# Optimization experiments

Measured on AMD Instinct MI355X. Metric: run time of the kernel, lower is better.

Reference implementation:

```python
import jax, jax.numpy as jnp
import numpy as np

N, E, IN, HID, OUT = 40000, 640000, 128, 512, 256


def setup_inputs() -> dict:
    key = jax.random.key(0)
    ks = jax.random.split(key, 8)
    x = jax.random.normal(ks[0], (N, IN), dtype=jnp.float32)
    edge_index = jax.random.randint(ks[1], (2, E), 0, N, dtype=jnp.int64)
    # SAGEConv params: lin_l (applied to aggregated neighbors, with bias),
    # lin_r (applied to root nodes, no bias) -- PyG defaults.
    def lin(k, fin, fout):
        return jax.random.normal(k, (fin, fout), dtype=jnp.float32) / np.sqrt(fin)
    return {
        "x": x,
        "edge_index": edge_index,
        "W1l": lin(ks[2], IN, HID),
        "b1": jnp.zeros((HID,), jnp.float32),
        "W1r": lin(ks[3], IN, HID),
        "W2l": lin(ks[4], HID, OUT),
        "b2": jnp.zeros((OUT,), jnp.float32),
        "W2r": lin(ks[5], HID, OUT),
    }


def _sage_conv(x, src, dst, Wl, b, Wr):
    n = x.shape[0]
    # gather messages from source nodes, mean-aggregate at destination
    msg = x[src]                                            # [E, F]
    agg = jax.ops.segment_sum(msg, dst, num_segments=n)     # [N, F]
    cnt = jax.ops.segment_sum(jnp.ones((src.shape[0],), x.dtype), dst,
                              num_segments=n)               # [N]
    agg = agg / jnp.maximum(cnt, 1.0)[:, None]
    # out = lin_l(mean_neighbors) + lin_r(x)
    return agg @ Wl + b + x @ Wr


def reference(x, edge_index, W1l, b1, W1r, W2l, b2, W2r):
    src, dst = edge_index[0], edge_index[1]
    h = jax.nn.relu(_sage_conv(x, src, dst, W1l, b1, W1r))
    return _sage_conv(h, src, dst, W2l, b2, W2r)
```

## Files before the change

kernel.cpp:

```cpp
#include <hip/hip_runtime.h>


#define N_NODES 40000
#define N_EDGES 640000
#define F_IN 128
#define F_HID 512
#define F_OUT 256
#define NB_SCAN 157

typedef unsigned short ushort_t;
typedef __attribute__((ext_vector_type(8))) short bf16x8;
typedef __attribute__((ext_vector_type(4))) float floatx4;

__device__ __forceinline__ ushort_t f2bf(float f) {
  union { float f; unsigned int u; } x; x.f = f;
  unsigned int r = (x.u + 0x7FFFu + ((x.u >> 16) & 1u)) >> 16;
  return (ushort_t)r;
}
__device__ __forceinline__ float bf2f(ushort_t u) {
  union { unsigned int u; float f; } x; x.u = ((unsigned int)u) << 16;
  return x.f;
}

__global__ void deg_kernel(const int* __restrict__ ei, int* __restrict__ deg) {
  int e = blockIdx.x * blockDim.x + threadIdx.x;
  if (e < N_EDGES) atomicAdd(&deg[ei[N_EDGES + e]], 1);
}

__global__ void scanA_kernel(const int* __restrict__ deg, int* __restrict__ bsum) {
  __shared__ int sdata[256];
  int i = blockIdx.x * 256 + threadIdx.x;
  sdata[threadIdx.x] = (i < N_NODES) ? deg[i] : 0;
  __syncthreads();
  #pragma unroll
  for (int off = 128; off > 0; off >>= 1) {
    if (threadIdx.x < off) sdata[threadIdx.x] += sdata[threadIdx.x + off];
    __syncthreads();
  }
  if (threadIdx.x == 0) bsum[blockIdx.x] = sdata[0];
}

__global__ void scanB_kernel(const int* __restrict__ bsum, int* __restrict__ boff) {
  __shared__ int buf[2][256];
  int tid = threadIdx.x;
  int v = (tid < NB_SCAN) ? bsum[tid] : 0;
  buf[0][tid] = v;
  __syncthreads();
  int cur = 0;
  #pragma unroll
  for (int off = 1; off < 256; off <<= 1) {
    int val = buf[cur][tid];
    if (tid >= off) val += buf[cur][tid - off];
    buf[cur ^ 1][tid] = val;
    __syncthreads();
    cur ^= 1;
  }
  if (tid < NB_SCAN) boff[tid] = buf[cur][tid] - v;
}

__global__ void scanC_kernel(const int* __restrict__ deg, const int* __restrict__ boff,
                             int* __restrict__ rowptr, int* __restrict__ cursor) {
  __shared__ int buf[2][256];
  int tid = threadIdx.x;
  int i = blockIdx.x * 256 + tid;
  int v = (i < N_NODES) ? deg[i] : 0;
  buf[0][tid] = v;
  __syncthreads();
  int cur = 0;
  #pragma unroll
  for (int off = 1; off < 256; off <<= 1) {
    int val = buf[cur][tid];
    if (tid >= off) val += buf[cur][tid - off];
    buf[cur ^ 1][tid] = val;
    __syncthreads();
    cur ^= 1;
  }
  if (i < N_NODES) {
    int ex = boff[blockIdx.x] + buf[cur][tid] - v;
    rowptr[i] = ex;
    cursor[i] = ex;
    if (i == N_NODES - 1) rowptr[N_NODES] = ex + v;
  }
}

__global__ void fill_kernel(const int* __restrict__ ei, int* __restrict__ cursor,
                            int* __restrict__ col) {
  int e = blockIdx.x * blockDim.x + threadIdx.x;
  if (e < N_EDGES) {
    int d = ei[N_EDGES + e];
    int s = ei[e];
    int pos = atomicAdd(&cursor[d], 1);
    col[pos] = s;
  }
}

__global__ void cvt_x_kernel(const float* __restrict__ x, ushort_t* __restrict__ xb) {
  int i = blockIdx.x * blockDim.x + threadIdx.x;
  const int n4 = (N_NODES * F_IN) / 4;
  if (i < n4) {
    float4 v = ((const float4*)x)[i];
    ushort4 o;
    o.x = f2bf(v.x); o.y = f2bf(v.y); o.z = f2bf(v.z); o.w = f2bf(v.w);
    ((ushort4*)xb)[i] = o;
  }
}

__global__ void wt_kernel(const float* __restrict__ W, ushort_t* __restrict__ Wt,
                          int K, int N, int rowoff, int koff, int ldt) {
  int i = blockIdx.x * blockDim.x + threadIdx.x;
  if (i < K * N) {
    int n = i / K, k = i - n * K;
    Wt[(size_t)(rowoff + n) * ldt + koff + k] = f2bf(W[(size_t)k * N + n]);
  }
}

__global__ void biascat_kernel(const float* __restrict__ b2, float* __restrict__ bc) {
  int i = threadIdx.x + blockIdx.x * blockDim.x;
  if (i < 512) bc[i] = (i < 256) ? 0.f : b2[i - 256];
}

__global__ void agg1_kernel(const ushort_t* __restrict__ Xb, ushort_t* __restrict__ Yb,
                            const int* __restrict__ rowptr, const int* __restrict__ colidx) {
  __shared__ int cols[64];
  int n = blockIdx.x, f = threadIdx.x;
  int s = rowptr[n], e = rowptr[n + 1];
  float s0 = 0.f, s1 = 0.f;
  for (int base = s; base < e; base += 64) {
    int cnt = min(64, e - base);
    __syncthreads();
    if (f < cnt) cols[f] = colidx[base + f];
    __syncthreads();
    for (int j = 0; j < cnt; ++j) {
      unsigned int v = *(const unsigned int*)(Xb + (size_t)cols[j] * F_IN + 2 * f);
      s0 += bf2f((ushort_t)(v & 0xffffu));
      s1 += bf2f((ushort_t)(v >> 16));
    }
  }
  float inv = 1.f / fmaxf((float)(e - s), 1.f);
  unsigned int o = (unsigned int)f2bf(s0 * inv) | ((unsigned int)f2bf(s1 * inv) << 16);
  *(unsigned int*)(Yb + (size_t)n * F_IN + 2 * f) = o;
}

__global__ void agg2_kernel(const ushort_t* __restrict__ hl, const float* __restrict__ hr,
                            float* __restrict__ out,
                            const int* __restrict__ rowptr, const int* __restrict__ colidx) {
  __shared__ int cols[128];
  int n = blockIdx.x, f = threadIdx.x;
  int s = rowptr[n], e = rowptr[n + 1];
  float s0 = 0.f, s1 = 0.f;
  for (int base = s; base < e; base += 128) {
    int cnt = min(128, e - base);
    __syncthreads();
    if (f < cnt) cols[f] = colidx[base + f];
    __syncthreads();
    for (int j = 0; j < cnt; ++j) {
      unsigned int v = *(const unsigned int*)(hl + (size_t)cols[j] * F_OUT + 2 * f);
      s0 += bf2f((ushort_t)(v & 0xffffu));
      s1 += bf2f((ushort_t)(v >> 16));
    }
  }
  float inv = 1.f / fmaxf((float)(e - s), 1.f);
  float2 hrv = *(const float2*)(hr + (size_t)n * F_OUT + 2 * f);
  float2 o;
  o.x = s0 * inv + hrv.x;
  o.y = s1 * inv + hrv.y;
  *(float2*)(out + (size_t)n * F_OUT + 2 * f) = o;
}

template <bool TWOPAIR, bool RELU, bool BIAS, bool OUT_BF16, bool SPLITOUT, int KT>
__global__ __launch_bounds__(256) void gemm_mfma(
    const ushort_t* __restrict__ A0, const ushort_t* __restrict__ A1,
    const ushort_t* __restrict__ Wt, const float* __restrict__ bias,
    float* __restrict__ Cf, ushort_t* __restrict__ Cb, int M) {
  const int BM = 64, BN = 256, BK = 32;
  const int NKC = KT / 8;
  __shared__ ushort_t Apan[64 * KT];
  __shared__ ushort_t Bt[BN * BK];
  const int tid = threadIdx.x;
  const int wave = tid >> 6, lane = tid & 63;
  const int lm = lane & 15, qk = lane >> 4;
  const int bn = blockIdx.x * BN;
  const int bm = blockIdx.y * BM;
  const int K0 = TWOPAIR ? KT / 2 : KT;
  const int K0c = K0 / 8;

  #pragma unroll
  for (int q = 0; q < (64 * NKC) / 256; ++q) {
    int c = tid + q * 256;
    int kc = c & (NKC - 1);
    int row = c / NKC;
    const ushort_t* src = (TWOPAIR && kc >= K0c)
        ? A1 + (size_t)(bm + row) * K0 + (kc - K0c) * 8
        : A0 + (size_t)(bm + row) * K0 + kc * 8;
    bf16x8 v = *(const bf16x8*)src;
    *(bf16x8*)(Apan + ((size_t)kc * 64 + row) * 8) = v;
  }

  floatx4 acc[4][4] = {};
  for (int kb = 0; kb < KT; kb += BK) {
    #pragma unroll
    for (int q = 0; q < 4; ++q) {
      int c = q * 256 + wave * 64 + lane;
      int n = c >> 2, kc2 = c & 3;
      const ushort_t* gb = Wt + (size_t)(bn + n) * KT + kb + kc2 * 8;
      ushort_t* lb = Bt + (size_t)(q * 256 + wave * 64) * 8;
      __builtin_amdgcn_global_load_lds(
          (const __attribute__((address_space(1))) void*)gb,
          (__attribute__((address_space(3))) void*)lb, 16, 0, 0);
    }
    __syncthreads();
    bf16x8 av[4], bv[4];
    #pragma unroll
    for (int mi = 0; mi < 4; ++mi)
      av[mi] = *(const bf16x8*)(Apan + ((size_t)(kb / 8 + qk) * 64 + mi * 16 + lm) * 8);
    #pragma unroll
    for (int ni = 0; ni < 4; ++ni)
      bv[ni] = *(const bf16x8*)(Bt + (size_t)(wave * 64 + ni * 16 + lm) * 32 + qk * 8);
    #pragma unroll
    for (int mi = 0; mi < 4; ++mi)
      #pragma unroll
      for (int ni = 0; ni < 4; ++ni)
        acc[mi][ni] = __builtin_amdgcn_mfma_f32_16x16x32_bf16(
            bv[ni], av[mi], acc[mi][ni], 0, 0, 0);
    __syncthreads();
  }

  #pragma unroll
  for (int ni = 0; ni < 4; ++ni) {
    int colg = bn + wave * 64 + ni * 16 + qk * 4;
    float4 b4 = {0.f, 0.f, 0.f, 0.f};
    if (BIAS) b4 = *(const float4*)&bias[colg];
    #pragma unroll
    for (int mi = 0; mi < 4; ++mi) {
      int rowg = bm + mi * 16 + lm;
      float v0 = acc[mi][ni][0] + b4.x;
      float v1 = acc[mi][ni][1] + b4.y;
      float v2 = acc[mi][ni][2] + b4.z;
      float v3 = acc[mi][ni][3] + b4.w;
      if (RELU) {
        v0 = fmaxf(v0, 0.f); v1 = fmaxf(v1, 0.f);
        v2 = fmaxf(v2, 0.f); v3 = fmaxf(v3, 0.f);
      }
      if (SPLITOUT) {
        if (colg < 256) {
          ushort4 o = {f2bf(v0), f2bf(v1), f2bf(v2), f2bf(v3)};
          *(ushort4*)&Cb[(size_t)rowg * 256 + colg] = o;
        } else {
          float4 o = {v0, v1, v2, v3};
          *(float4*)&Cf[(size_t)rowg * 256 + (colg - 256)] = o;
        }
      } else if (OUT_BF16) {
        ushort4 o = {f2bf(v0), f2bf(v1), f2bf(v2), f2bf(v3)};
        *(ushort4*)&Cb[(size_t)rowg * 512 + colg] = o;
      } else {
        float4 o = {v0, v1, v2, v3};
        *(float4*)&Cf[(size_t)rowg * 512 + colg] = o;
      }
    }
  }
}

extern "C" void kernel_launch(void* const* d_in, const int* in_sizes, int n_in,
                              void* d_out, int out_size, void* d_ws, size_t ws_size,
                              hipStream_t stream) {
  const float* x = (const float*)d_in[0];
  const int* ei = (const int*)d_in[1];
  const float* W1l = (const float*)d_in[2];
  const float* b1 = (const float*)d_in[3];
  const float* W1r = (const float*)d_in[4];
  const float* W2l = (const float*)d_in[5];
  const float* b2 = (const float*)d_in[6];
  const float* W2r = (const float*)d_in[7];
  float* out = (float*)d_out;

  char* ws = (char*)d_ws;
  size_t off = 0;
  auto alloc = [&](size_t bytes) {
    void* p = ws + off;
    off = (off + bytes + 255) & ~(size_t)255;
    return p;
  };
  int* deg = (int*)alloc((size_t)N_NODES * 4);
  int* rowptr = (int*)alloc((size_t)(N_NODES + 1) * 4);
  int* cursor = (int*)alloc((size_t)N_NODES * 4);
  int* col = (int*)alloc((size_t)N_EDGES * 4);
  int* bsum = (int*)alloc((size_t)NB_SCAN * 4);
  int* boff = (int*)alloc((size_t)NB_SCAN * 4);
  ushort_t* x_bf = (ushort_t*)alloc((size_t)N_NODES * F_IN * 2);
  ushort_t* aggx_bf = (ushort_t*)alloc((size_t)N_NODES * F_IN * 2);
  ushort_t* h_bf = (ushort_t*)alloc((size_t)N_NODES * F_HID * 2);
  ushort_t* hl_bf = (ushort_t*)alloc((size_t)N_NODES * F_OUT * 2);
  float* hr = (float*)alloc((size_t)N_NODES * F_OUT * 4);
  ushort_t* Wcat1t = (ushort_t*)alloc((size_t)512 * 256 * 2);
  ushort_t* Wcatt = (ushort_t*)alloc((size_t)512 * F_HID * 2);
  float* biascat = (float*)alloc(512 * 4);

  hipMemsetAsync(deg, 0, (size_t)N_NODES * 4, stream);
  deg_kernel<<<(N_EDGES + 255) / 256, 256, 0, stream>>>(ei, deg);
  scanA_kernel<<<NB_SCAN, 256, 0, stream>>>(deg, bsum);
  scanB_kernel<<<1, 256, 0, stream>>>(bsum, boff);
  scanC_kernel<<<NB_SCAN, 256, 0, stream>>>(deg, boff, rowptr, cursor);
  fill_kernel<<<(N_EDGES + 255) / 256, 256, 0, stream>>>(ei, cursor, col);

  cvt_x_kernel<<<(N_NODES * F_IN / 4 + 255) / 256, 256, 0, stream>>>(x, x_bf);
  wt_kernel<<<(F_IN * F_HID + 255) / 256, 256, 0, stream>>>(W1l, Wcat1t, 128, 512, 0, 0, 256);
  wt_kernel<<<(F_IN * F_HID + 255) / 256, 256, 0, stream>>>(W1r, Wcat1t, 128, 512, 0, 128, 256);
  wt_kernel<<<(F_HID * F_OUT + 255) / 256, 256, 0, stream>>>(W2l, Wcatt, 512, 256, 0, 0, 512);
  wt_kernel<<<(F_HID * F_OUT + 255) / 256, 256, 0, stream>>>(W2r, Wcatt, 512, 256, 256, 0, 512);
  biascat_kernel<<<2, 256, 0, stream>>>(b2, biascat);

  agg1_kernel<<<N_NODES, 64, 0, stream>>>(x_bf, aggx_bf, rowptr, col);
  gemm_mfma<true, true, true, true, false, 256>
      <<<dim3(2, N_NODES / 64), 256, 0, stream>>>(
          aggx_bf, x_bf, Wcat1t, b1, nullptr, h_bf, N_NODES);

  gemm_mfma<false, false, true, false, true, 512>
      <<<dim3(2, N_NODES / 64), 256, 0, stream>>>(
          h_bf, nullptr, Wcatt, biascat, hr, hl_bf, N_NODES);
  agg2_kernel<<<N_NODES, 128, 0, stream>>>(hl_bf, hr, out, rowptr, col);
}
```

Before: 329.0 us.

## Load GEMM weight tiles straight into registers and swizzle the A panel in LDS

The MFMA GEMM no longer stages weight (B) tiles in shared memory through global_load_lds with two barriers per K step. Each wave now reads its B fragments directly from global memory into two register sets, prefetching the next 32-wide slice while the current one feeds the MFMAs, and the K loop is unrolled by 64. The A panel in LDS is stored with an XOR swizzle to cut bank conflicts, and a single barrier after the panel fill replaces the per-iteration syncs. In exchange, register pressure rises and B reads are no longer shared across waves through LDS, so global and L2 traffic for weights goes up.

```diff
diff --git a/kernel.cpp b/kernel.cpp
--- a/kernel.cpp
+++ b/kernel.cpp
@@ -172,10 +172,9 @@
     const ushort_t* __restrict__ A0, const ushort_t* __restrict__ A1,
     const ushort_t* __restrict__ Wt, const float* __restrict__ bias,
     float* __restrict__ Cf, ushort_t* __restrict__ Cb, int M) {
-  const int BM = 64, BN = 256, BK = 32;
+  const int BM = 64, BN = 256;
   const int NKC = KT / 8;
   __shared__ ushort_t Apan[64 * KT];
-  __shared__ ushort_t Bt[BN * BK];
   const int tid = threadIdx.x;
   const int wave = tid >> 6, lane = tid & 63;
   const int lm = lane & 15, qk = lane >> 4;
@@ -193,36 +192,57 @@
         ? A1 + (size_t)(bm + row) * K0 + (kc - K0c) * 8
         : A0 + (size_t)(bm + row) * K0 + kc * 8;
     bf16x8 v = *(const bf16x8*)src;
-    *(bf16x8*)(Apan + ((size_t)kc * 64 + row) * 8) = v;
-  }
+    size_t off = ((size_t)(kc * 64 + row) * 16) ^ (size_t)((kc & 7) << 4);
+    *(bf16x8*)((char*)Apan + off) = v;
+  }
+
+  const ushort_t* bp = Wt + (size_t)(bn + wave * 64 + lm) * KT + qk * 8;
+  bf16x8 bvA[4], bvB[4];
+  #pragma unroll
+  for (int ni = 0; ni < 4; ++ni)
+    bvA[ni] = *(const bf16x8*)(bp + (size_t)ni * 16 * KT);
+
+  __syncthreads();
 
   floatx4 acc[4][4] = {};
-  for (int kb = 0; kb < KT; kb += BK) {
-    #pragma unroll
-    for (int q = 0; q < 4; ++q) {
-      int c = q * 256 + wave * 64 + lane;
-      int n = c >> 2, kc2 = c & 3;
-      const ushort_t* gb = Wt + (size_t)(bn + n) * KT + kb + kc2 * 8;
-      ushort_t* lb = Bt + (size_t)(q * 256 + wave * 64) * 8;
-      __builtin_amdgcn_global_load_lds(
-          (const __attribute__((address_space(1))) void*)gb,
-          (__attribute__((address_space(3))) void*)lb, 16, 0, 0);
-    }
-    __syncthreads();
-    bf16x8 av[4], bv[4];
-    #pragma unroll
-    for (int mi = 0; mi < 4; ++mi)
-      av[mi] = *(const bf16x8*)(Apan + ((size_t)(kb / 8 + qk) * 64 + mi * 16 + lm) * 8);
+  #pragma unroll 1
+  for (int kb = 0; kb < KT; kb += 64) {
     #pragma unroll
     for (int ni = 0; ni < 4; ++ni)
-      bv[ni] = *(const bf16x8*)(Bt + (size_t)(wave * 64 + ni * 16 + lm) * 32 + qk * 8);
+      bvB[ni] = *(const bf16x8*)(bp + (size_t)ni * 16 * KT + kb + 32);
+
+    bf16x8 av[4];
+    const int kc0 = kb / 8 + qk;
+    #pragma unroll
+    for (int mi = 0; mi < 4; ++mi) {
+      size_t off = ((size_t)(kc0 * 64 + mi * 16 + lm) * 16) ^ (size_t)((kc0 & 7) << 4);
+      av[mi] = *(const bf16x8*)((char*)Apan + off);
+    }
     #pragma unroll
     for (int mi = 0; mi < 4; ++mi)
       #pragma unroll
       for (int ni = 0; ni < 4; ++ni)
         acc[mi][ni] = __builtin_amdgcn_mfma_f32_16x16x32_bf16(
-            bv[ni], av[mi], acc[mi][ni], 0, 0, 0);
-    __syncthreads();
+            bvA[ni], av[mi], acc[mi][ni], 0, 0, 0);
+
+    if (kb + 64 < KT) {
+      #pragma unroll
+      for (int ni = 0; ni < 4; ++ni)
+        bvA[ni] = *(const bf16x8*)(bp + (size_t)ni * 16 * KT + kb + 64);
+    }
+
+    const int kc1 = kb / 8 + 4 + qk;
+    #pragma unroll
+    for (int mi = 0; mi < 4; ++mi) {
+      size_t off = ((size_t)(kc1 * 64 + mi * 16 + lm) * 16) ^ (size_t)((kc1 & 7) << 4);
+      av[mi] = *(const bf16x8*)((char*)Apan + off);
+    }
+    #pragma unroll
+    for (int mi = 0; mi < 4; ++mi)
+      #pragma unroll
+      for (int ni = 0; ni < 4; ++ni)
+        acc[mi][ni] = __builtin_amdgcn_mfma_f32_16x16x32_bf16(
+            bvB[ni], av[mi], acc[mi][ni], 0, 0, 0);
   }
 
   #pragma unroll
```

New measurement: 339.4 us. 1.03x slower.
